# Optimization experiments

Measured on AMD Instinct MI355X. Metric: run time of the kernel, lower is better.

The kernel has to match this reference:

```python
import jax, jax.numpy as jnp
import numpy as np

B, K, T, C = 4, 8, 2048, 64

def setup_inputs() -> dict:
    key = jax.random.key(0)
    ks = jax.random.split(key, 7)
    return {
        "x": jax.random.normal(ks[0], (B, K, T, C), dtype=jnp.float32),
        "Wq": jax.random.normal(ks[1], (C, C), dtype=jnp.float32) / np.sqrt(C),
        "bq": jax.random.normal(ks[2], (C,), dtype=jnp.float32) * 0.01,
        "Wk": jax.random.normal(ks[3], (C, C), dtype=jnp.float32) / np.sqrt(C),
        "bk": jax.random.normal(ks[4], (C,), dtype=jnp.float32) * 0.01,
        "Wv": jax.random.normal(ks[5], (C, C), dtype=jnp.float32) / np.sqrt(C),
        "bv": jax.random.normal(ks[6], (C,), dtype=jnp.float32) * 0.01,
    }

def reference(x, Wq, bq, Wk, bk, Wv, bv):
    c_dim = x.shape[-1]
    # torch nn.Linear: y = x @ W.T + b
    q = jnp.einsum('bktc,dc->bktd', x, Wq) + bq
    k = jnp.einsum('bktc,dc->bktd', x, Wk) + bk
    v = jnp.einsum('bktc,dc->bktd', x, Wv) + bv
    scores = jnp.einsum('bkic,bkjc->bkij', q, k) / jnp.sqrt(jnp.float32(c_dim))
    attn = jax.nn.softmax(scores, axis=-1)
    out = jnp.einsum('bkij,bkjc->bkic', attn, v)
    return out
```

## Files before the change

kernel.cpp:

```cpp
#include <hip/hip_runtime.h>


#define T_DIM 2048
#define NHEAD 32
#define NKT   (T_DIM / 64)
#define HSTRIDE (T_DIM * 64)
#define QSCALE 0.18033688011112042f
#define SOFF  8.0f

#define SWZ(row, grp) ((row) * 64 + ((((grp) ^ ((row) & 7)) & 7) * 8))

typedef _Float16 h8 __attribute__((ext_vector_type(8)));
typedef _Float16 h4 __attribute__((ext_vector_type(4)));
typedef __fp16   g2 __attribute__((ext_vector_type(2)));
typedef float    f4 __attribute__((ext_vector_type(4)));

union H4U { h4 v; g2 p[2]; };
union H8U { h8 v; h4 h[2]; };

#if defined(__has_builtin)
#if __has_builtin(__builtin_amdgcn_exp2f)
#define EXP2(x) __builtin_amdgcn_exp2f(x)
#endif
#endif
#ifndef EXP2
__device__ inline float exp2_raw(float x) {
    float r;
    asm("v_exp_f32 %0, %1" : "=v"(r) : "v"(x));
    return r;
}
#define EXP2(x) exp2_raw(x)
#endif

__device__ inline h4 cvt4(f4 x) {
    H4U u;
    u.p[0] = __builtin_amdgcn_cvt_pkrtz(x[0], x[1]);
    u.p[1] = __builtin_amdgcn_cvt_pkrtz(x[2], x[3]);
    return u.v;
}

__global__ __launch_bounds__(256) void qkv_proj_kernel(
    const float* __restrict__ x,
    const float* __restrict__ Wq, const float* __restrict__ bq,
    const float* __restrict__ Wk, const float* __restrict__ bk,
    const float* __restrict__ Wv, const float* __restrict__ bv,
    _Float16* __restrict__ qh, _Float16* __restrict__ khT,
    _Float16* __restrict__ vtT)
{
    __shared__ _Float16 ws[3][64 * 64];
    __shared__ _Float16 xs[64 * 64];
    __shared__ float bsh[3][64];
    _Float16* ot = xs;

    const int tid  = threadIdx.x;
    const int row0 = blockIdx.x * 64;
    const int head = blockIdx.x >> 5;
    const int t0   = (blockIdx.x & 31) * 64;

    #pragma unroll
    for (int m = 0; m < 3; ++m) {
        const float* Wm = (m == 0) ? Wq : ((m == 1) ? Wk : Wv);
        const float* bm = (m == 0) ? bq : ((m == 1) ? bk : bv);
        #pragma unroll
        for (int pass = 0; pass < 4; ++pass) {
            const int idx = pass * 1024 + tid * 4;
            const int d = idx >> 6, c = idx & 63;
            f4 wv = *(const f4*)(Wm + idx);
            *(h4*)&ws[m][SWZ(d, c >> 3) + (c & 7)] = cvt4(wv);
        }
        if (tid < 64) bsh[m][tid] = bm[tid];
    }
    {
        const float* xb = x + (size_t)row0 * 64;
        #pragma unroll
        for (int pass = 0; pass < 4; ++pass) {
            const int idx = pass * 1024 + tid * 4;
            const int r = idx >> 6, c = idx & 63;
            f4 xv = *(const f4*)(xb + idx);
            *(h4*)&xs[SWZ(r, c >> 3) + (c & 7)] = cvt4(xv);
        }
    }
    __syncthreads();

    const int w    = tid >> 6;
    const int lane = tid & 63;
    const int l15  = lane & 15;
    const int qd   = lane >> 4;

    h8 af[2];
    #pragma unroll
    for (int ch = 0; ch < 2; ++ch)
        af[ch] = *(const h8*)&xs[SWZ(w * 16 + l15, ch * 4 + qd)];

    #pragma unroll
    for (int m = 0; m < 3; ++m) {
        h8 bf[4][2];
        #pragma unroll
        for (int ns = 0; ns < 4; ++ns)
            #pragma unroll
            for (int ch = 0; ch < 2; ++ch)
                bf[ns][ch] = *(const h8*)&ws[m][SWZ(ns * 16 + l15, ch * 4 + qd)];

        f4 acc[4];
        #pragma unroll
        for (int ns = 0; ns < 4; ++ns)
            acc[ns] = (f4){0.f, 0.f, 0.f, 0.f};
        #pragma unroll
        for (int ch = 0; ch < 2; ++ch)
            #pragma unroll
            for (int ns = 0; ns < 4; ++ns)
                acc[ns] = __builtin_amdgcn_mfma_f32_16x16x32_f16(
                    af[ch], bf[ns][ch], acc[ns], 0, 0, 0);

        __syncthreads();
        if (m < 2) {
            #pragma unroll
            for (int ns = 0; ns < 4; ++ns) {
                const int d = ns * 16 + l15;
                const float bias = bsh[m][d];
                #pragma unroll
                for (int r = 0; r < 4; ++r) {
                    const int t = w * 16 + qd * 4 + r;
                    float v = acc[ns][r] + bias;
                    if (m == 0) v *= QSCALE;
                    ot[SWZ(t, d >> 3) + (d & 7)] = (_Float16)v;
                }
            }
            __syncthreads();
            if (m == 0) {
                #pragma unroll
                for (int pass = 0; pass < 2; ++pass) {
                    const int t  = pass * 32 + (tid >> 3);
                    const int c0 = (tid & 7) * 8;
                    *(h8*)&qh[(size_t)(row0 + t) * 64 + c0] =
                        *(const h8*)&ot[SWZ(t, tid & 7)];
                }
            } else {
                #pragma unroll
                for (int pass = 0; pass < 2; ++pass) {
                    const int f    = pass * 2048 + tid * 8;
                    const int Jl   = f >> 10;
                    const int rest = f & 1023;
                    const int ch_  = rest >> 9;
                    const int qd_  = (rest >> 7) & 3;
                    const int l15_ = (rest >> 3) & 15;
                    h8 val = *(const h8*)&ot[SWZ(Jl * 16 + l15_, ch_ * 4 + qd_)];
                    *(h8*)&khT[(size_t)head * HSTRIDE + ((t0 >> 4) + Jl) * 1024 + rest] = val;
                }
            }
        } else {
            #pragma unroll
            for (int ns = 0; ns < 4; ++ns) {
                const int d = ns * 16 + l15;
                const float bias = bsh[2][d];
                const int tl = w * 16 + qd * 4;
                f4 pvf;
                #pragma unroll
                for (int r = 0; r < 4; ++r)
                    pvf[r] = acc[ns][r] + bias;
                *(h4*)&ot[SWZ(d, tl >> 3) + (tl & 7)] = cvt4(pvf);
            }
            __syncthreads();
            #pragma unroll
            for (int pass = 0; pass < 2; ++pass) {
                const int f   = pass * 2048 + tid * 8;
                const int jbl = f >> 8;
                const int c0  = (f >> 2) & 63;
                const int jl  = jbl * 4;
                H8U val;
                val.h[0] = *(const h4*)&ot[SWZ(c0,     jl >> 3) + (jl & 7)];
                val.h[1] = *(const h4*)&ot[SWZ(c0 + 1, jl >> 3) + (jl & 7)];
                *(h8*)&vtT[(size_t)head * HSTRIDE + ((t0 >> 2) + jbl) * 256 + c0 * 4] = val.v;
            }
        }
    }
}

__global__ __launch_bounds__(256, 2) void attn_kernel(
    const _Float16* __restrict__ qh, const _Float16* __restrict__ khT,
    const _Float16* __restrict__ vtT, float* __restrict__ out)
{
    const int tid  = threadIdx.x;
    const int w    = tid >> 6;
    const int lane = tid & 63;
    const int l15  = lane & 15;
    const int qd   = lane >> 4;

    const int bid   = blockIdx.x;
    const int xcd   = bid & 7;
    const int slot  = bid >> 3;
    const int head  = xcd * 4 + (slot >> 4);
    const int qpart = slot & 15;
    const int q0    = qpart * 128 + w * 32;

    h8 qf[2][2];
    #pragma unroll
    for (int is = 0; is < 2; ++is) {
        const _Float16* qp = qh + (size_t)(head * T_DIM + q0 + is * 16 + l15) * 64 + qd * 8;
        qf[is][0] = *(const h8*)qp;
        qf[is][1] = *(const h8*)(qp + 32);
    }

    const h4 vones = {(_Float16)1.0f, (_Float16)1.0f, (_Float16)1.0f, (_Float16)1.0f};
    f4 lacc[2] = {(f4){0.f,0.f,0.f,0.f}, (f4){0.f,0.f,0.f,0.f}};
    f4 oacc[2][4];
    #pragma unroll
    for (int is = 0; is < 2; ++is)
        #pragma unroll
        for (int cs = 0; cs < 4; ++cs)
            oacc[is][cs] = (f4){0.f, 0.f, 0.f, 0.f};

    const _Float16* kA = khT + (size_t)head * HSTRIDE;
    const _Float16* kB = kA + 2048;
    const _Float16* vA = vtT + (size_t)head * HSTRIDE;
    const _Float16* vB = vA + 2048;
    const int ko = lane * 8;
    const int vo = qd * 256 + l15 * 4;

    h8 kf[4][2];
    #pragma unroll
    for (int jt = 0; jt < 4; ++jt)
        #pragma unroll
        for (int ch = 0; ch < 2; ++ch)
            kf[jt][ch] = *(const h8*)(((jt < 2) ? kA : kB) + (jt & 1) * 1024 + ch * 512 + ko);

    for (int kt = 0; kt < NKT; ++kt) {
        h4 vf[4][4];
        #pragma unroll
        for (int jt = 0; jt < 4; ++jt)
            #pragma unroll
            for (int cs = 0; cs < 4; ++cs)
                vf[jt][cs] = *(const h4*)(((jt < 2) ? vA : vB) + (jt & 1) * 1024 + cs * 64 + vo);

        f4 st[4][2];
        #pragma unroll
        for (int jt = 0; jt < 4; ++jt)
            #pragma unroll
            for (int is = 0; is < 2; ++is)
                st[jt][is] = (f4){-SOFF, -SOFF, -SOFF, -SOFF};
        #pragma unroll
        for (int ch = 0; ch < 2; ++ch)
            #pragma unroll
            for (int jt = 0; jt < 4; ++jt)
                #pragma unroll
                for (int is = 0; is < 2; ++is)
                    st[jt][is] = __builtin_amdgcn_mfma_f32_16x16x32_f16(
                        kf[jt][ch], qf[is][ch], st[jt][is], 0, 0, 0);

        kA += 4096; kB += 4096;
        if (kt + 1 < NKT) {
            #pragma unroll
            for (int jt = 0; jt < 4; ++jt)
                #pragma unroll
                for (int ch = 0; ch < 2; ++ch)
                    kf[jt][ch] = *(const h8*)(((jt < 2) ? kA : kB) + (jt & 1) * 1024 + ch * 512 + ko);
        }

        h4 pf[4][2];
        #pragma unroll
        for (int is = 0; is < 2; ++is)
            #pragma unroll
            for (int jt = 0; jt < 4; ++jt) {
                f4 p;
                p[0] = EXP2(st[jt][is][0]);
                p[1] = EXP2(st[jt][is][1]);
                p[2] = EXP2(st[jt][is][2]);
                p[3] = EXP2(st[jt][is][3]);
                pf[jt][is] = cvt4(p);
            }

        #pragma unroll
        for (int jt = 0; jt < 4; ++jt) {
            #pragma unroll
            for (int cs = 0; cs < 4; ++cs)
                #pragma unroll
                for (int is = 0; is < 2; ++is)
                    oacc[is][cs] = __builtin_amdgcn_mfma_f32_16x16x16f16(
                        pf[jt][is], vf[jt][cs], oacc[is][cs], 0, 0, 0);
            #pragma unroll
            for (int is = 0; is < 2; ++is)
                lacc[is] = __builtin_amdgcn_mfma_f32_16x16x16f16(
                    pf[jt][is], vones, lacc[is], 0, 0, 0);
        }
        vA += 4096; vB += 4096;
    }

    #pragma unroll
    for (int is = 0; is < 2; ++is) {
        float linv[4];
        #pragma unroll
        for (int r = 0; r < 4; ++r)
            linv[r] = 1.f / lacc[is][r];
        #pragma unroll
        for (int cs = 0; cs < 4; ++cs) {
            const int c = cs * 16 + l15;
            #pragma unroll
            for (int r = 0; r < 4; ++r) {
                const int t = q0 + is * 16 + qd * 4 + r;
                out[(size_t)(head * T_DIM + t) * 64 + c] = oacc[is][cs][r] * linv[r];
            }
        }
    }
}

extern "C" void kernel_launch(void* const* d_in, const int* in_sizes, int n_in,
                              void* d_out, int out_size, void* d_ws, size_t ws_size,
                              hipStream_t stream)
{
    (void)in_sizes; (void)n_in; (void)out_size; (void)ws_size;
    const float* x  = (const float*)d_in[0];
    const float* Wq = (const float*)d_in[1];
    const float* bq = (const float*)d_in[2];
    const float* Wk = (const float*)d_in[3];
    const float* bk = (const float*)d_in[4];
    const float* Wv = (const float*)d_in[5];
    const float* bv = (const float*)d_in[6];
    float* out = (float*)d_out;

    _Float16* qh  = (_Float16*)d_ws;
    _Float16* khT = qh + (size_t)NHEAD * HSTRIDE;
    _Float16* vtT = khT + (size_t)NHEAD * HSTRIDE;

    hipLaunchKernelGGL(qkv_proj_kernel, dim3(1024), dim3(256), 0, stream,
                       x, Wq, bq, Wk, bk, Wv, bv, qh, khT, vtT);
    hipLaunchKernelGGL(attn_kernel, dim3(512), dim3(256), 0, stream,
                       qh, khT, vtT, out);
}
```

Baseline: 140.3 us.

## Split key range across wave pairs and merge partial softmax sums via LDS

The attention kernel now gives each pair of waves the same 32 queries and splits the 2048 keys in half, one half per wave. Partial output and row-sum accumulators from the second wave go through shared memory and are added in by the first, and the grid doubles to 1024 blocks. The V layout written by the projection kernel changes so each lane loads two contiguous 8-wide fp16 vectors per column slice instead of four 4-wide loads. This adds parallelism and shortens each wave's serial loop, at the cost of a block barrier, an LDS merge, and half the waves sitting idle during the final store.

```diff
diff --git a/kernel.cpp b/kernel.cpp
--- a/kernel.cpp
+++ b/kernel.cpp
@@ -3,7 +3,6 @@
 
 #define T_DIM 2048
 #define NHEAD 32
-#define NKT   (T_DIM / 64)
 #define HSTRIDE (T_DIM * 64)
 #define QSCALE 0.18033688011112042f
 #define SOFF  8.0f
@@ -164,13 +163,16 @@
             #pragma unroll
             for (int pass = 0; pass < 2; ++pass) {
                 const int f   = pass * 2048 + tid * 8;
-                const int jbl = f >> 8;
-                const int c0  = (f >> 2) & 63;
-                const int jl  = jbl * 4;
+                const int qd3 = f >> 10;
+                const int rem = f & 1023;
+                const int c   = rem >> 4;
+                const int g   = (rem & 15) >> 3;
+                const int ta  = (2 * g) * 16 + qd3 * 4;
+                const int tb  = ta + 16;
                 H8U val;
-                val.h[0] = *(const h4*)&ot[SWZ(c0,     jl >> 3) + (jl & 7)];
-                val.h[1] = *(const h4*)&ot[SWZ(c0 + 1, jl >> 3) + (jl & 7)];
-                *(h8*)&vtT[(size_t)head * HSTRIDE + ((t0 >> 2) + jbl) * 256 + c0 * 4] = val.v;
+                val.h[0] = *(const h4*)&ot[SWZ(c, ta >> 3) + (ta & 7)];
+                val.h[1] = *(const h4*)&ot[SWZ(c, tb >> 3) + (tb & 7)];
+                *(h8*)&vtT[(size_t)head * HSTRIDE + (t0 >> 6) * 4096 + f] = val.v;
             }
         }
     }
@@ -180,18 +182,20 @@
     const _Float16* __restrict__ qh, const _Float16* __restrict__ khT,
     const _Float16* __restrict__ vtT, float* __restrict__ out)
 {
+    __shared__ float mrg[2][64][41];
     const int tid  = threadIdx.x;
     const int w    = tid >> 6;
     const int lane = tid & 63;
     const int l15  = lane & 15;
     const int qd   = lane >> 4;
-
-    const int bid   = blockIdx.x;
-    const int xcd   = bid & 7;
-    const int slot  = bid >> 3;
-    const int head  = xcd * 4 + (slot >> 4);
-    const int qpart = slot & 15;
-    const int q0    = qpart * 128 + w * 32;
+    const int qgrp = w >> 1;
+    const int kph  = w & 1;
+
+    const int bid  = blockIdx.x;
+    const int xcd  = bid & 7;
+    const int slot = bid >> 3;
+    const int head = xcd * 4 + (slot >> 5);
+    const int q0   = (slot & 31) * 64 + qgrp * 32;
 
     h8 qf[2][2];
     #pragma unroll
@@ -210,12 +214,11 @@
         for (int cs = 0; cs < 4; ++cs)
             oacc[is][cs] = (f4){0.f, 0.f, 0.f, 0.f};
 
-    const _Float16* kA = khT + (size_t)head * HSTRIDE;
+    const _Float16* kA = khT + (size_t)head * HSTRIDE + kph * 65536;
     const _Float16* kB = kA + 2048;
-    const _Float16* vA = vtT + (size_t)head * HSTRIDE;
-    const _Float16* vB = vA + 2048;
+    const _Float16* vA = vtT + (size_t)head * HSTRIDE + kph * 65536;
     const int ko = lane * 8;
-    const int vo = qd * 256 + l15 * 4;
+    const int vo = qd * 1024 + l15 * 16;
 
     h8 kf[4][2];
     #pragma unroll
@@ -224,13 +227,13 @@
         for (int ch = 0; ch < 2; ++ch)
             kf[jt][ch] = *(const h8*)(((jt < 2) ? kA : kB) + (jt & 1) * 1024 + ch * 512 + ko);
 
-    for (int kt = 0; kt < NKT; ++kt) {
-        h4 vf[4][4];
-        #pragma unroll
-        for (int jt = 0; jt < 4; ++jt)
-            #pragma unroll
-            for (int cs = 0; cs < 4; ++cs)
-                vf[jt][cs] = *(const h4*)(((jt < 2) ? vA : vB) + (jt & 1) * 1024 + cs * 64 + vo);
+    for (int kt = 0; kt < 16; ++kt) {
+        H8U vf8[4][2];
+        #pragma unroll
+        for (int cs = 0; cs < 4; ++cs) {
+            vf8[cs][0].v = *(const h8*)(vA + cs * 256 + vo);
+            vf8[cs][1].v = *(const h8*)(vA + cs * 256 + vo + 8);
+        }
 
         f4 st[4][2];
         #pragma unroll
@@ -248,7 +251,7 @@
                         kf[jt][ch], qf[is][ch], st[jt][is], 0, 0, 0);
 
         kA += 4096; kB += 4096;
-        if (kt + 1 < NKT) {
+        if (kt < 15) {
             #pragma unroll
             for (int jt = 0; jt < 4; ++jt)
                 #pragma unroll
@@ -276,28 +279,45 @@
                 #pragma unroll
                 for (int is = 0; is < 2; ++is)
                     oacc[is][cs] = __builtin_amdgcn_mfma_f32_16x16x16f16(
-                        pf[jt][is], vf[jt][cs], oacc[is][cs], 0, 0, 0);
+                        pf[jt][is], vf8[cs][jt >> 1].h[jt & 1], oacc[is][cs], 0, 0, 0);
             #pragma unroll
             for (int is = 0; is < 2; ++is)
                 lacc[is] = __builtin_amdgcn_mfma_f32_16x16x16f16(
                     pf[jt][is], vones, lacc[is], 0, 0, 0);
         }
-        vA += 4096; vB += 4096;
-    }
-
-    #pragma unroll
-    for (int is = 0; is < 2; ++is) {
-        float linv[4];
-        #pragma unroll
-        for (int r = 0; r < 4; ++r)
-            linv[r] = 1.f / lacc[is][r];
-        #pragma unroll
-        for (int cs = 0; cs < 4; ++cs) {
-            const int c = cs * 16 + l15;
-            #pragma unroll
-            for (int r = 0; r < 4; ++r) {
-                const int t = q0 + is * 16 + qd * 4 + r;
-                out[(size_t)(head * T_DIM + t) * 64 + c] = oacc[is][cs][r] * linv[r];
+        vA += 4096;
+    }
+
+    if (kph == 1) {
+        #pragma unroll
+        for (int is = 0; is < 2; ++is) {
+            #pragma unroll
+            for (int cs = 0; cs < 4; ++cs)
+                #pragma unroll
+                for (int r = 0; r < 4; ++r)
+                    mrg[qgrp][lane][(is * 4 + cs) * 4 + r] = oacc[is][cs][r];
+            #pragma unroll
+            for (int r = 0; r < 4; ++r)
+                mrg[qgrp][lane][32 + is * 4 + r] = lacc[is][r];
+        }
+    }
+    __syncthreads();
+    if (kph == 0) {
+        #pragma unroll
+        for (int is = 0; is < 2; ++is) {
+            float linv[4];
+            #pragma unroll
+            for (int r = 0; r < 4; ++r)
+                linv[r] = 1.f / (lacc[is][r] + mrg[qgrp][lane][32 + is * 4 + r]);
+            #pragma unroll
+            for (int cs = 0; cs < 4; ++cs) {
+                const int c = cs * 16 + l15;
+                #pragma unroll
+                for (int r = 0; r < 4; ++r) {
+                    const int t = q0 + is * 16 + qd * 4 + r;
+                    float o = oacc[is][cs][r] + mrg[qgrp][lane][(is * 4 + cs) * 4 + r];
+                    out[(size_t)(head * T_DIM + t) * 64 + c] = o * linv[r];
+                }
             }
         }
     }
@@ -323,6 +343,6 @@
 
     hipLaunchKernelGGL(qkv_proj_kernel, dim3(1024), dim3(256), 0, stream,
                        x, Wq, bq, Wk, bk, Wv, bv, qh, khT, vtT);
-    hipLaunchKernelGGL(attn_kernel, dim3(512), dim3(256), 0, stream,
+    hipLaunchKernelGGL(attn_kernel, dim3(1024), dim3(256), 0, stream,
                        qh, khT, vtT, out);
 }
```

After: 131.0 us. 1.07x faster.
